# Kernel optimization log

Hardware: AMD Instinct MI355X
Metric: run time of the kernel (lower is better)

Reference implementation:

```python
import jax, jax.numpy as jnp
import numpy as np

B, N = 2048, 110
H1, F1 = 5, 24   # gat1: 5 heads, 24-dim, concat
H2, F2 = 3, 3    # gat2: 3 heads, 3-dim, average
NEG = -9e15
ALPHA = 0.2  # tf.nn.leaky_relu default alpha


def _glorot(key, shape):
    fan_in, fan_out = shape[-2], shape[-1]
    lim = np.sqrt(6.0 / (fan_in + fan_out))
    return jax.random.uniform(key, shape, jnp.float32, -lim, lim)


def setup_inputs() -> dict:
    key = jax.random.key(0)
    ks = jax.random.split(key, 12)
    X = jax.random.normal(ks[0], (B, N, N), jnp.float32)
    # sparse-ish 0/1 adjacency with self-loops
    A = (jax.random.uniform(ks[1], (B, N, N)) < 0.3).astype(jnp.float32)
    A = jnp.maximum(A, jnp.eye(N, dtype=jnp.float32)[None])
    return {
        "X": X,
        "A": A,
        "M": jax.random.normal(ks[2], (N, N), jnp.float32),  # learnable mask
        "W1": _glorot(ks[3], (H1, N, F1)),
        "as1": _glorot(ks[4], (H1, F1, 1))[..., 0],
        "an1": _glorot(ks[5], (H1, F1, 1))[..., 0],
        "b1": jnp.zeros((F1,), jnp.float32),
        "W2": _glorot(ks[6], (H2, H1 * F1, F2)),
        "as2": _glorot(ks[7], (H2, F2, 1))[..., 0],
        "an2": _glorot(ks[8], (H2, F2, 1))[..., 0],
        "b2": jnp.zeros((F2,), jnp.float32),
        "fc1_w": _glorot(ks[9], (F2, 1)),
        "fc2_w": _glorot(ks[10], (N, N)),
    }


def _gat_layer(X, A, W, a_s, a_n, b, concat):
    # X: [B,N,Din]; W: [H,Din,F]; a_s,a_n: [H,F]; b: [F]
    feats = jnp.einsum('bni,hif->bhnf', X, W)               # per-head projection
    e_s = jnp.einsum('bhnf,hf->bhn', feats, a_s)
    e_n = jnp.einsum('bhnf,hf->bhn', feats, a_n)
    e = jax.nn.leaky_relu(e_s[..., :, None] + e_n[..., None, :], ALPHA)  # [B,H,N,N]
    e = jnp.where(A[:, None] > 0.0, e, NEG)                  # adjacency mask
    attn = jax.nn.softmax(e, axis=-1)
    h = jnp.einsum('bhnm,bhmf->bhnf', attn, feats) + b       # aggregate + bias
    if concat:
        h = jax.nn.leaky_relu(h, ALPHA)
        b_, hh, n_, f_ = h.shape
        return h.transpose(0, 2, 1, 3).reshape(b_, n_, hh * f_)
    # 'average': add heads / H, then activation
    return jax.nn.leaky_relu(h.mean(axis=1), ALPHA)


def reference(X, A, M, W1, as1, an1, b1, W2, as2, an2, b2, fc1_w, fc2_w):
    Xm = X * jax.nn.sigmoid(M)[None]                         # learnable mask gating
    h1 = _gat_layer(Xm, A, W1, as1, an1, b1, concat=True)    # [B,N,H1*F1]
    h2 = _gat_layer(h1, A, W2, as2, an2, b2, concat=False)   # [B,N,F2]
    node_prob = jax.nn.sigmoid(h2 @ fc1_w)                   # [B,N,1]
    t = node_prob.reshape(-1, N)                             # [B,N]
    attn_prob = jax.nn.softmax(t @ fc2_w, axis=-1)           # [B,N]
    return jnp.sum(t * attn_prob, axis=1, keepdims=True)     # [B,1]
```

## Files before the change

### kernel.cpp

```cpp
#include <hip/hip_runtime.h>
#include <math.h>

#define NB 2048
#define NV 110
#define NH1 5
#define NF1 24
#define NH2 3
#define NF2 3
#define C1 (NH1*NF1)
#define LALPHA 0.2f

constexpr int NN = NV*NV;
constexpr int T1 = 512;
constexpr int KP = 136;
constexpr int W1ROWS = 144;

typedef _Float16 f16;
typedef f16  f16x8 __attribute__((ext_vector_type(8)));
typedef f16  f16x4 __attribute__((ext_vector_type(4)));
typedef __fp16 h16x2 __attribute__((ext_vector_type(2)));
typedef float f32x4 __attribute__((ext_vector_type(4)));

__device__ __forceinline__ f32x4 mfma16(f16x8 a, f16x8 b, f32x4 c) {
  return __builtin_amdgcn_mfma_f32_16x16x32_f16(a, b, c, 0, 0, 0);
}
__device__ __forceinline__ float lrelu(float x){ return x > 0.f ? x : LALPHA*x; }
__device__ __forceinline__ float frcp(float x){ return __builtin_amdgcn_rcpf(x); }
__device__ __forceinline__ float sigm(float x){ return frcp(1.f+__expf(-x)); }
__device__ __forceinline__ float expm4(float v){
  return __builtin_amdgcn_exp2f(fmaf(v, 1.442695041f, -5.770780163f));
}
__device__ __forceinline__ float wmax(float v){
  #pragma unroll
  for (int d=32; d; d>>=1) v = fmaxf(v, __shfl_xor(v,d));
  return v;
}
__device__ __forceinline__ float wsum(float v){
  #pragma unroll
  for (int d=32; d; d>>=1) v += __shfl_xor(v,d);
  return v;
}
__device__ __forceinline__ f32x4 ld4u(const float* p){
  f32x4 v; __builtin_memcpy(&v, p, 16); return v;
}

__global__ void precomp_kernel(const float* __restrict__ M, const float* __restrict__ W1,
                               const float* __restrict__ as1, const float* __restrict__ an1,
                               const float* __restrict__ W2, const float* __restrict__ as2,
                               const float* __restrict__ an2, const float* __restrict__ fc2w,
                               float* __restrict__ Msig, f16* __restrict__ W1tg,
                               f16* __restrict__ W2tg, f16* __restrict__ fc2tg) {
  const int i = blockIdx.x*256 + threadIdx.x;
  if (i < NN) {
    Msig[i] = sigm(M[i]);
  } else if (i < NN + W1ROWS*KP) {
    const int j = i - NN, f = j/KP, k = j%KP;
    float v = 0.f;
    if (k < NV) {
      if (f < C1) {
        v = W1[(f/NF1)*(NV*NF1) + k*NF1 + (f%NF1)];
      } else if (f >= 128 && f < 133) {
        const int h = f - 128;
        for (int ff = 0; ff < NF1; ++ff)
          v += W1[h*(NV*NF1) + k*NF1 + ff] * as1[h*NF1 + ff];
      } else if (f >= 133 && f < 138) {
        const int h = f - 133;
        for (int ff = 0; ff < NF1; ++ff)
          v += W1[h*(NV*NF1) + k*NF1 + ff] * an1[h*NF1 + ff];
      }
    }
    W1tg[f*KP + k] = (f16)v;
  } else if (i < NN + W1ROWS*KP + 16*KP) {
    const int j = i - NN - W1ROWS*KP, r = j/KP, k = j%KP;
    float v = 0.f;
    if (k < C1) {
      if (r < 9) {
        v = W2[(r/NF2)*(C1*NF2) + k*NF2 + (r%NF2)];
      } else if (r < 12) {
        const int g = r - 9;
        for (int f2 = 0; f2 < NF2; ++f2)
          v += W2[g*(C1*NF2) + k*NF2 + f2] * as2[g*NF2 + f2];
      } else if (r < 15) {
        const int g = r - 12;
        for (int f2 = 0; f2 < NF2; ++f2)
          v += W2[g*(C1*NF2) + k*NF2 + f2] * an2[g*NF2 + f2];
      }
    }
    W2tg[r*KP + k] = (f16)v;
  } else if (i < NN + W1ROWS*KP + 16*KP + 112*KP) {
    const int j = i - NN - W1ROWS*KP - 16*KP, col = j/KP, k = j%KP;
    float v = 0.f;
    if (col < NV && k < NV) v = fc2w[k*NV + col];
    fc2tg[col*KP + k] = (f16)v;
  }
}

__global__ __launch_bounds__(T1, 4) void gat_fused(
  const float* __restrict__ X, const float* __restrict__ A,
  const float* __restrict__ Msig, const f16* __restrict__ W1tg,
  const float* __restrict__ b1,  const f16* __restrict__ W2tg,
  const float* __restrict__ b2,  const float* __restrict__ fc1w,
  const f16* __restrict__ fc2tg, float* __restrict__ out)
{
  __shared__ __attribute__((aligned(16))) f16 sXm [112*KP];
  __shared__ __attribute__((aligned(16))) f16 sFt [128*KP];
  __shared__ __attribute__((aligned(16))) f16 sF2t[16*KP];
  __shared__ __attribute__((aligned(16))) float sES [NH1*112];
  __shared__ __attribute__((aligned(16))) float sEN [NH1*128];
  __shared__ __attribute__((aligned(16))) float sES2[NH2*112];
  __shared__ __attribute__((aligned(16))) float sEN2[NH2*128];
  __shared__ unsigned long long sAM[2*112];

  const int b = blockIdx.x, tid = threadIdx.x;
  const int wv = tid >> 6, lane = tid & 63;
  const int lr = lane & 15, lh = lane >> 4;
  const float* __restrict__ Xb = X + (size_t)b*NN;
  const float* __restrict__ Ab = A + (size_t)b*NN;

  float* const sT = sES;
  float* const sS = sES + 128;

  for (int n = tid; n < 110; n += T1) {
    *(unsigned*)&sXm[n*KP + 110] = 0u;
    *(uint4*)&sXm[n*KP + 112] = uint4{0,0,0,0};
    *(uint4*)&sXm[n*KP + 120] = uint4{0,0,0,0};
    *(uint4*)&sXm[n*KP + 128] = uint4{0,0,0,0};
  }
  for (int i = tid; i < 2*KP/8; i += T1)
    ((uint4*)&sXm[110*KP])[i] = uint4{0,0,0,0};
  for (int n = tid; n < 128; n += T1) {
    *(uint4*)&sFt[n*KP + 112] = uint4{0,0,0,0};
    *(uint4*)&sFt[n*KP + 120] = uint4{0,0,0,0};
    *(uint4*)&sFt[n*KP + 128] = uint4{0,0,0,0};
  }
  for (int i = tid; i < (16*KP)/8; i += T1)
    ((uint4*)sF2t)[i] = uint4{0,0,0,0};
  if (tid < 4) sAM[220 + tid] = 0ull;

  for (int t = tid; t < NV*28; t += T1) {
    const int n = t/28, c = t%28, k = 4*c;
    if (c < 27) {
      f32x4 x = ld4u(Xb + n*NV + k);
      f32x4 m = ld4u(Msig + n*NV + k);
      union { f16x4 v4; h16x2 h2[2]; } u;
      u.h2[0] = __builtin_amdgcn_cvt_pkrtz(x[0]*m[0], x[1]*m[1]);
      u.h2[1] = __builtin_amdgcn_cvt_pkrtz(x[2]*m[2], x[3]*m[3]);
      *(f16x4*)&sXm[n*KP + k] = u.v4;
    } else {
      sXm[n*KP + 108] = (f16)(Xb[n*NV+108]*Msig[n*NV+108]);
      sXm[n*KP + 109] = (f16)(Xb[n*NV+109]*Msig[n*NV+109]);
    }
  }
  #pragma unroll
  for (int i = 0; i < 14; ++i) {
    const int n = wv + 8*i;
    if (n < NV) {
      unsigned long long m0 = __ballot(Ab[n*NV + lane] > 0.f);
      const int mm = 64 + lane;
      unsigned long long m1 = __ballot((mm < NV) && (Ab[n*NV + mm] > 0.f));
      if (lane == 0) { sAM[2*n] = m0; sAM[2*n+1] = m1; }
    }
  }
  f16x8 bW[4], bL[4];
  #pragma unroll
  for (int k = 0; k < 4; ++k)
    bW[k] = *(const f16x8*)&W1tg[(wv*16 + lr)*KP + k*32 + lh*8];
  if (wv < 2) {
    #pragma unroll
    for (int k = 0; k < 4; ++k)
      bL[k] = *(const f16x8*)&W1tg[(128 + lr)*KP + k*32 + lh*8];
  }
  __syncthreads();

  #pragma unroll
  for (int m = 0; m < 7; ++m) {
    f32x4 acc = {0.f,0.f,0.f,0.f};
    #pragma unroll
    for (int k = 0; k < 4; ++k) {
      f16x8 af = *(const f16x8*)&sXm[(m*16 + lr)*KP + k*32 + lh*8];
      acc = mfma16(af, bW[k], acc);
    }
    f16x4 v;
    #pragma unroll
    for (int r = 0; r < 4; ++r) v[r] = (f16)acc[r];
    *(f16x4*)&sFt[(wv*16 + lr)*KP + m*16 + lh*4] = v;
  }
  if (wv < 2) {
    const int mlo = wv ? 4 : 0, mhi = wv ? 7 : 4;
    for (int m = mlo; m < mhi; ++m) {
      f32x4 acc = {0.f,0.f,0.f,0.f};
      #pragma unroll
      for (int k = 0; k < 4; ++k) {
        f16x8 af = *(const f16x8*)&sXm[(m*16 + lr)*KP + k*32 + lh*8];
        acc = mfma16(af, bL[k], acc);
      }
      const int mg0 = m*16 + lh*4;
      if (lr < 5)       *(f32x4*)&sES[lr*112 + mg0] = acc;
      else if (lr < 10) *(f32x4*)&sEN[(lr-5)*128 + mg0] = acc;
    }
  }
  __syncthreads();

  const int row  = wv*16 + lr;
  const int arow = (row < 112) ? row : 0;
  const unsigned long long am0 = sAM[2*arow], am1 = sAM[2*arow+1];
  const float bvt0 = (lr < NF1) ? b1[lr] : 0.f;
  const float bvt1 = (16 + lr < NF1) ? b1[16 + lr] : 0.f;

  f16 h1r[5][2][4];
  f16x8 pa[4];
  if (wv < 7) {
    #pragma unroll
    for (int p = 0; p < 5; ++p) {
      const float es = sES[p*112 + row];
      float psum = 0.f;
      #pragma unroll
      for (int k = 0; k < 4; ++k) {
        const int cb = k*32 + lh*8;
        const f32x4 enA = *(const f32x4*)&sEN[p*128 + cb];
        const f32x4 enB = *(const f32x4*)&sEN[p*128 + cb + 4];
        const unsigned bits = (unsigned)(((cb & 64) ? am1 : am0) >> (cb & 63)) & 0xFFu;
        float e[8];
        #pragma unroll
        for (int j = 0; j < 8; ++j) {
          float v = es + ((j < 4) ? enA[j] : enB[j-4]);
          v = fmaxf(v, LALPHA*v);
          v = (bits & (1u << j)) ? v : -1e30f;
          e[j] = expm4(v);
        }
        psum += ((e[0]+e[1]) + (e[2]+e[3])) + ((e[4]+e[5]) + (e[6]+e[7]));
        union { f16x8 v8; h16x2 h2[4]; } u;
        u.h2[0] = __builtin_amdgcn_cvt_pkrtz(e[0], e[1]);
        u.h2[1] = __builtin_amdgcn_cvt_pkrtz(e[2], e[3]);
        u.h2[2] = __builtin_amdgcn_cvt_pkrtz(e[4], e[5]);
        u.h2[3] = __builtin_amdgcn_cvt_pkrtz(e[6], e[7]);
        pa[k] = u.v8;
      }
      psum += __shfl_xor(psum, 16);
      psum += __shfl_xor(psum, 32);
      f32x4 rs;
      #pragma unroll
      for (int r = 0; r < 4; ++r) rs[r] = __shfl(psum, lh*4 + r);
      #pragma unroll
      for (int nt2 = 0; nt2 < 2; ++nt2) {
        f32x4 acc = {0.f,0.f,0.f,0.f};
        #pragma unroll
        for (int k = 0; k < 4; ++k) {
          f16x8 bf = *(const f16x8*)&sFt[(p*NF1 + nt2*16 + lr)*KP + k*32 + lh*8];
          acc = mfma16(pa[k], bf, acc);
        }
        const float bv = nt2 ? bvt1 : bvt0;
        #pragma unroll
        for (int r = 0; r < 4; ++r)
          h1r[p][nt2][r] = (f16)lrelu(acc[r]*frcp(rs[r]) + bv);
      }
    }
    #pragma unroll
    for (int p = 0; p < 5; ++p) {
      #pragma unroll
      for (int nt2 = 0; nt2 < 2; ++nt2) {
        const int fl = nt2*16 + lr;
        if (fl < NF1) {
          #pragma unroll
          for (int r = 0; r < 4; ++r) {
            const int mg = wv*16 + lh*4 + r;
            if (mg < NV) sXm[mg*KP + p*NF1 + fl] = h1r[p][nt2][r];
          }
        }
      }
    }
    {
      f32x4 acc = {0.f,0.f,0.f,0.f};
      #pragma unroll
      for (int k = 0; k < 4; ++k) {
        f16x8 af = *(const f16x8*)&sXm[(wv*16 + lr)*KP + k*32 + lh*8];
        f16x8 bf = *(const f16x8*)&W2tg[lr*KP + k*32 + lh*8];
        acc = mfma16(af, bf, acc);
      }
      const int mg0 = wv*16 + lh*4;
      if (lr < 9) {
        #pragma unroll
        for (int r = 0; r < 4; ++r) {
          const int mg = mg0 + r;
          if (mg < NV) sF2t[lr*KP + mg] = (f16)acc[r];
        }
      } else if (lr < 12) {
        *(f32x4*)&sES2[(lr-9)*112 + mg0] = acc;
      } else if (lr < 15) {
        *(f32x4*)&sEN2[(lr-12)*128 + mg0] = acc;
      }
    }
  }
  __syncthreads();

  f32x4 a2_0 = {0.f,0.f,0.f,0.f};
  f32x4 a2_1 = {0.f,0.f,0.f,0.f};
  f32x4 a2_2 = {0.f,0.f,0.f,0.f};
  float ps0 = 0.f, ps1 = 0.f, ps2 = 0.f;
  if (wv == 7) {
    if (lane < 18) sT[110 + lane] = 0.f;
  }
  if (wv < 7) {
    #pragma unroll
    for (int g = 0; g < 3; ++g) {
      const float es = sES2[g*112 + row];
      float psum = 0.f;
      #pragma unroll
      for (int k = 0; k < 4; ++k) {
        const int cb = k*32 + lh*8;
        const f32x4 enA = *(const f32x4*)&sEN2[g*128 + cb];
        const f32x4 enB = *(const f32x4*)&sEN2[g*128 + cb + 4];
        const unsigned bits = (unsigned)(((cb & 64) ? am1 : am0) >> (cb & 63)) & 0xFFu;
        float e[8];
        #pragma unroll
        for (int j = 0; j < 8; ++j) {
          float v = es + ((j < 4) ? enA[j] : enB[j-4]);
          v = fmaxf(v, LALPHA*v);
          v = (bits & (1u << j)) ? v : -1e30f;
          e[j] = expm4(v);
        }
        psum += ((e[0]+e[1]) + (e[2]+e[3])) + ((e[4]+e[5]) + (e[6]+e[7]));
        union { f16x8 v8; h16x2 h2[4]; } u;
        u.h2[0] = __builtin_amdgcn_cvt_pkrtz(e[0], e[1]);
        u.h2[1] = __builtin_amdgcn_cvt_pkrtz(e[2], e[3]);
        u.h2[2] = __builtin_amdgcn_cvt_pkrtz(e[4], e[5]);
        u.h2[3] = __builtin_amdgcn_cvt_pkrtz(e[6], e[7]);
        pa[k] = u.v8;
      }
      psum += __shfl_xor(psum, 16);
      psum += __shfl_xor(psum, 32);
      if (g == 0) ps0 = psum; else if (g == 1) ps1 = psum; else ps2 = psum;
      const int brow = (lr < NF2) ? (g*NF2 + lr) : 15;
      #pragma unroll
      for (int k = 0; k < 4; ++k) {
        f16x8 bf = *(const f16x8*)&sF2t[brow*KP + k*32 + lh*8];
        if (g == 0)      a2_0 = mfma16(pa[k], bf, a2_0);
        else if (g == 1) a2_1 = mfma16(pa[k], bf, a2_1);
        else             a2_2 = mfma16(pa[k], bf, a2_2);
      }
    }
    const float fcv = (lr < NF2) ? fc1w[lr] : 0.f;
    const float b2v = (lr < NF2) ? b2[lr]  : 0.f;
    #pragma unroll
    for (int r = 0; r < 4; ++r) {
      const int src = lh*4 + r;
      const float rs0 = __shfl(ps0, src);
      const float rs1 = __shfl(ps1, src);
      const float rs2 = __shfl(ps2, src);
      const float hsum = a2_0[r]*frcp(rs0) + a2_1[r]*frcp(rs1)
                       + a2_2[r]*frcp(rs2);
      float hv = (lr < NF2) ? lrelu(hsum*(1.f/NH2) + b2v)*fcv : 0.f;
      hv += __shfl_xor(hv, 1);
      hv += __shfl_xor(hv, 2);
      hv += __shfl_xor(hv, 4);
      hv += __shfl_xor(hv, 8);
      if (lr == 0) {
        const int mg = wv*16 + lh*4 + r;
        if (mg < NV) sT[mg] = sigm(hv);
      }
    }
  }
  __syncthreads();
  if (wv < 7) {
    f32x4 acc = {0.f,0.f,0.f,0.f};
    #pragma unroll
    for (int k = 0; k < 4; ++k) {
      const int cb = k*32 + lh*8;
      const f32x4 tA = *(const f32x4*)&sT[cb];
      const f32x4 tB = *(const f32x4*)&sT[cb + 4];
      union { f16x8 v8; h16x2 h2[4]; } u;
      u.h2[0] = __builtin_amdgcn_cvt_pkrtz(tA[0], tA[1]);
      u.h2[1] = __builtin_amdgcn_cvt_pkrtz(tA[2], tA[3]);
      u.h2[2] = __builtin_amdgcn_cvt_pkrtz(tB[0], tB[1]);
      u.h2[3] = __builtin_amdgcn_cvt_pkrtz(tB[2], tB[3]);
      f16x8 bf = *(const f16x8*)&fc2tg[(wv*16 + lr)*KP + k*32 + lh*8];
      acc = mfma16(u.v8, bf, acc);
    }
    const int col = wv*16 + lr;
    if (lh == 0 && col < NV) sS[col] = acc[0];
  }
  __syncthreads();
  if (wv == 0) {
    const float s0 = sS[lane];
    const float s1 = (64+lane < NV) ? sS[64+lane] : -1e38f;
    const float mx = wmax(fmaxf(s0, s1));
    const float p0 = __expf(s0 - mx);
    const float p1 = (64+lane < NV) ? __expf(s1 - mx) : 0.f;
    const float sum = wsum(p0 + p1);
    float val = sT[lane]*p0 + ((64+lane < NV) ? sT[64+lane]*p1 : 0.f);
    val = wsum(val);
    if (lane == 0) out[b] = val*frcp(sum);
  }
}

extern "C" void kernel_launch(void* const* d_in, const int* in_sizes, int n_in,
                              void* d_out, int out_size, void* d_ws, size_t ws_size,
                              hipStream_t stream) {
  const float* X   = (const float*)d_in[0];
  const float* A   = (const float*)d_in[1];
  const float* M   = (const float*)d_in[2];
  const float* W1  = (const float*)d_in[3];
  const float* as1 = (const float*)d_in[4];
  const float* an1 = (const float*)d_in[5];
  const float* b1  = (const float*)d_in[6];
  const float* W2  = (const float*)d_in[7];
  const float* as2 = (const float*)d_in[8];
  const float* an2 = (const float*)d_in[9];
  const float* b2  = (const float*)d_in[10];
  const float* fc1 = (const float*)d_in[11];
  const float* fc2 = (const float*)d_in[12];
  float* out = (float*)d_out;

  float* Msig = (float*)d_ws;
  f16* W1tg  = (f16*)((char*)d_ws + 48400);
  f16* W2tg  = (f16*)((char*)d_ws + 48400 + W1ROWS*KP*2);
  f16* fc2tg = (f16*)((char*)d_ws + 48400 + W1ROWS*KP*2 + 16*KP*2);

  const int pre_items = NN + W1ROWS*KP + 16*KP + 112*KP;
  precomp_kernel<<<(pre_items + 255)/256, 256, 0, stream>>>(
      M, W1, as1, an1, W2, as2, an2, fc2, Msig, W1tg, W2tg, fc2tg);
  gat_fused<<<NB, T1, 0, stream>>>(X, A, Msig, W1tg, b1, W2tg,
                                   b2, fc1, fc2tg, out);
}
```

Measured before the change: 150.0 us.

## Double block to 16 waves and split heads across two wave halves

Raises the block size from 512 to 1024 threads and splits the work between two groups of 8 waves. The first GEMM's row tiles, the layer-1 heads (3 vs 2) and the layer-2 heads (2 vs 1) are divided between the groups. Partial layer-2 head outputs go through a new shared buffer, and an extra barrier separates the layer-1 aggregation from the layer-2 projection. The goal is more parallelism per batch item with fewer serial head iterations per wave. The cost is extra synchronisation and register pressure at 1024 threads per block, and fewer resident blocks per CU.

```diff
diff --git a/kernel.cpp b/kernel.cpp
--- a/kernel.cpp
+++ b/kernel.cpp
@@ -11,7 +11,7 @@
 #define LALPHA 0.2f
 
 constexpr int NN = NV*NV;
-constexpr int T1 = 512;
+constexpr int T1 = 1024;
 constexpr int KP = 136;
 constexpr int W1ROWS = 144;
 
@@ -95,7 +95,7 @@
   }
 }
 
-__global__ __launch_bounds__(T1, 4) void gat_fused(
+__global__ __launch_bounds__(T1, 8) void gat_fused(
   const float* __restrict__ X, const float* __restrict__ A,
   const float* __restrict__ Msig, const f16* __restrict__ W1tg,
   const float* __restrict__ b1,  const f16* __restrict__ W2tg,
@@ -110,9 +110,11 @@
   __shared__ __attribute__((aligned(16))) float sES2[NH2*112];
   __shared__ __attribute__((aligned(16))) float sEN2[NH2*128];
   __shared__ unsigned long long sAM[2*112];
+  __shared__ __attribute__((aligned(16))) float sHP[112*4];
 
   const int b = blockIdx.x, tid = threadIdx.x;
   const int wv = tid >> 6, lane = tid & 63;
+  const int wq = wv & 7, half = wv >> 3;
   const int lr = lane & 15, lh = lane >> 4;
   const float* __restrict__ Xb = X + (size_t)b*NN;
   const float* __restrict__ Ab = A + (size_t)b*NN;
@@ -152,8 +154,8 @@
     }
   }
   #pragma unroll
-  for (int i = 0; i < 14; ++i) {
-    const int n = wv + 8*i;
+  for (int i = 0; i < 7; ++i) {
+    const int n = wv + 16*i;
     if (n < NV) {
       unsigned long long m0 = __ballot(Ab[n*NV + lane] > 0.f);
       const int mm = 64 + lane;
@@ -164,204 +166,221 @@
   f16x8 bW[4], bL[4];
   #pragma unroll
   for (int k = 0; k < 4; ++k)
-    bW[k] = *(const f16x8*)&W1tg[(wv*16 + lr)*KP + k*32 + lh*8];
-  if (wv < 2) {
+    bW[k] = *(const f16x8*)&W1tg[(wq*16 + lr)*KP + k*32 + lh*8];
+  if (half && wq < 7) {
     #pragma unroll
     for (int k = 0; k < 4; ++k)
       bL[k] = *(const f16x8*)&W1tg[(128 + lr)*KP + k*32 + lh*8];
   }
   __syncthreads();
 
-  #pragma unroll
-  for (int m = 0; m < 7; ++m) {
-    f32x4 acc = {0.f,0.f,0.f,0.f};
-    #pragma unroll
-    for (int k = 0; k < 4; ++k) {
-      f16x8 af = *(const f16x8*)&sXm[(m*16 + lr)*KP + k*32 + lh*8];
-      acc = mfma16(af, bW[k], acc);
-    }
-    f16x4 v;
-    #pragma unroll
-    for (int r = 0; r < 4; ++r) v[r] = (f16)acc[r];
-    *(f16x4*)&sFt[(wv*16 + lr)*KP + m*16 + lh*4] = v;
-  }
-  if (wv < 2) {
-    const int mlo = wv ? 4 : 0, mhi = wv ? 7 : 4;
+  {
+    const int mlo = half ? 4 : 0, mhi = half ? 7 : 4;
     for (int m = mlo; m < mhi; ++m) {
       f32x4 acc = {0.f,0.f,0.f,0.f};
       #pragma unroll
       for (int k = 0; k < 4; ++k) {
         f16x8 af = *(const f16x8*)&sXm[(m*16 + lr)*KP + k*32 + lh*8];
+        acc = mfma16(af, bW[k], acc);
+      }
+      f16x4 v;
+      #pragma unroll
+      for (int r = 0; r < 4; ++r) v[r] = (f16)acc[r];
+      *(f16x4*)&sFt[(wq*16 + lr)*KP + m*16 + lh*4] = v;
+    }
+    if (half && wq < 7) {
+      f32x4 acc = {0.f,0.f,0.f,0.f};
+      #pragma unroll
+      for (int k = 0; k < 4; ++k) {
+        f16x8 af = *(const f16x8*)&sXm[(wq*16 + lr)*KP + k*32 + lh*8];
         acc = mfma16(af, bL[k], acc);
       }
-      const int mg0 = m*16 + lh*4;
+      const int mg0 = wq*16 + lh*4;
       if (lr < 5)       *(f32x4*)&sES[lr*112 + mg0] = acc;
       else if (lr < 10) *(f32x4*)&sEN[(lr-5)*128 + mg0] = acc;
     }
   }
   __syncthreads();
 
-  const int row  = wv*16 + lr;
+  const int row  = wq*16 + lr;
   const int arow = (row < 112) ? row : 0;
   const unsigned long long am0 = sAM[2*arow], am1 = sAM[2*arow+1];
   const float bvt0 = (lr < NF1) ? b1[lr] : 0.f;
   const float bvt1 = (16 + lr < NF1) ? b1[16 + lr] : 0.f;
-
-  f16 h1r[5][2][4];
+  const int np = half ? 2 : 3, pbase = half ? 3 : 0;
+
+  f16 h1r[3][2][4];
   f16x8 pa[4];
-  if (wv < 7) {
-    #pragma unroll
-    for (int p = 0; p < 5; ++p) {
-      const float es = sES[p*112 + row];
-      float psum = 0.f;
-      #pragma unroll
-      for (int k = 0; k < 4; ++k) {
-        const int cb = k*32 + lh*8;
-        const f32x4 enA = *(const f32x4*)&sEN[p*128 + cb];
-        const f32x4 enB = *(const f32x4*)&sEN[p*128 + cb + 4];
-        const unsigned bits = (unsigned)(((cb & 64) ? am1 : am0) >> (cb & 63)) & 0xFFu;
-        float e[8];
-        #pragma unroll
-        for (int j = 0; j < 8; ++j) {
-          float v = es + ((j < 4) ? enA[j] : enB[j-4]);
-          v = fmaxf(v, LALPHA*v);
-          v = (bits & (1u << j)) ? v : -1e30f;
-          e[j] = expm4(v);
+  if (wq < 7) {
+    #pragma unroll
+    for (int pi = 0; pi < 3; ++pi) {
+      if (pi < np) {
+        const int p = pbase + pi;
+        const float es = sES[p*112 + row];
+        float psum = 0.f;
+        #pragma unroll
+        for (int k = 0; k < 4; ++k) {
+          const int cb = k*32 + lh*8;
+          const f32x4 enA = *(const f32x4*)&sEN[p*128 + cb];
+          const f32x4 enB = *(const f32x4*)&sEN[p*128 + cb + 4];
+          const unsigned bits = (unsigned)(((cb & 64) ? am1 : am0) >> (cb & 63)) & 0xFFu;
+          float e[8];
+          #pragma unroll
+          for (int j = 0; j < 8; ++j) {
+            float v = es + ((j < 4) ? enA[j] : enB[j-4]);
+            v = fmaxf(v, LALPHA*v);
+            v = (bits & (1u << j)) ? v : -1e30f;
+            e[j] = expm4(v);
+          }
+          psum += ((e[0]+e[1]) + (e[2]+e[3])) + ((e[4]+e[5]) + (e[6]+e[7]));
+          union { f16x8 v8; h16x2 h2[4]; } u;
+          u.h2[0] = __builtin_amdgcn_cvt_pkrtz(e[0], e[1]);
+          u.h2[1] = __builtin_amdgcn_cvt_pkrtz(e[2], e[3]);
+          u.h2[2] = __builtin_amdgcn_cvt_pkrtz(e[4], e[5]);
+          u.h2[3] = __builtin_amdgcn_cvt_pkrtz(e[6], e[7]);
+          pa[k] = u.v8;
         }
-        psum += ((e[0]+e[1]) + (e[2]+e[3])) + ((e[4]+e[5]) + (e[6]+e[7]));
-        union { f16x8 v8; h16x2 h2[4]; } u;
-        u.h2[0] = __builtin_amdgcn_cvt_pkrtz(e[0], e[1]);
-        u.h2[1] = __builtin_amdgcn_cvt_pkrtz(e[2], e[3]);
-        u.h2[2] = __builtin_amdgcn_cvt_pkrtz(e[4], e[5]);
-        u.h2[3] = __builtin_amdgcn_cvt_pkrtz(e[6], e[7]);
-        pa[k] = u.v8;
-      }
-      psum += __shfl_xor(psum, 16);
-      psum += __shfl_xor(psum, 32);
-      f32x4 rs;
-      #pragma unroll
-      for (int r = 0; r < 4; ++r) rs[r] = __shfl(psum, lh*4 + r);
-      #pragma unroll
-      for (int nt2 = 0; nt2 < 2; ++nt2) {
-        f32x4 acc = {0.f,0.f,0.f,0.f};
-        #pragma unroll
-        for (int k = 0; k < 4; ++k) {
-          f16x8 bf = *(const f16x8*)&sFt[(p*NF1 + nt2*16 + lr)*KP + k*32 + lh*8];
-          acc = mfma16(pa[k], bf, acc);
+        psum += __shfl_xor(psum, 16);
+        psum += __shfl_xor(psum, 32);
+        f32x4 rs;
+        #pragma unroll
+        for (int r = 0; r < 4; ++r) rs[r] = __shfl(psum, lh*4 + r);
+        #pragma unroll
+        for (int nt2 = 0; nt2 < 2; ++nt2) {
+          f32x4 acc = {0.f,0.f,0.f,0.f};
+          #pragma unroll
+          for (int k = 0; k < 4; ++k) {
+            f16x8 bf = *(const f16x8*)&sFt[(p*NF1 + nt2*16 + lr)*KP + k*32 + lh*8];
+            acc = mfma16(pa[k], bf, acc);
+          }
+          const float bv = nt2 ? bvt1 : bvt0;
+          #pragma unroll
+          for (int r = 0; r < 4; ++r)
+            h1r[pi][nt2][r] = (f16)lrelu(acc[r]*frcp(rs[r]) + bv);
         }
-        const float bv = nt2 ? bvt1 : bvt0;
-        #pragma unroll
-        for (int r = 0; r < 4; ++r)
-          h1r[p][nt2][r] = (f16)lrelu(acc[r]*frcp(rs[r]) + bv);
-      }
-    }
-    #pragma unroll
-    for (int p = 0; p < 5; ++p) {
-      #pragma unroll
-      for (int nt2 = 0; nt2 < 2; ++nt2) {
-        const int fl = nt2*16 + lr;
-        if (fl < NF1) {
-          #pragma unroll
-          for (int r = 0; r < 4; ++r) {
-            const int mg = wv*16 + lh*4 + r;
-            if (mg < NV) sXm[mg*KP + p*NF1 + fl] = h1r[p][nt2][r];
+      }
+    }
+    #pragma unroll
+    for (int pi = 0; pi < 3; ++pi) {
+      if (pi < np) {
+        const int p = pbase + pi;
+        #pragma unroll
+        for (int nt2 = 0; nt2 < 2; ++nt2) {
+          const int fl = nt2*16 + lr;
+          if (fl < NF1) {
+            #pragma unroll
+            for (int r = 0; r < 4; ++r) {
+              const int mg = wq*16 + lh*4 + r;
+              if (mg < NV) sXm[mg*KP + p*NF1 + fl] = h1r[pi][nt2][r];
+            }
           }
         }
       }
     }
-    {
-      f32x4 acc = {0.f,0.f,0.f,0.f};
+  }
+  __syncthreads();
+
+  if (!half && wq < 7) {
+    f32x4 acc = {0.f,0.f,0.f,0.f};
+    #pragma unroll
+    for (int k = 0; k < 4; ++k) {
+      f16x8 af = *(const f16x8*)&sXm[(wq*16 + lr)*KP + k*32 + lh*8];
+      f16x8 bf = *(const f16x8*)&W2tg[lr*KP + k*32 + lh*8];
+      acc = mfma16(af, bf, acc);
+    }
+    const int mg0 = wq*16 + lh*4;
+    if (lr < 9) {
       #pragma unroll
-      for (int k = 0; k < 4; ++k) {
-        f16x8 af = *(const f16x8*)&sXm[(wv*16 + lr)*KP + k*32 + lh*8];
-        f16x8 bf = *(const f16x8*)&W2tg[lr*KP + k*32 + lh*8];
-        acc = mfma16(af, bf, acc);
-      }
-      const int mg0 = wv*16 + lh*4;
-      if (lr < 9) {
-        #pragma unroll
-        for (int r = 0; r < 4; ++r) {
-          const int mg = mg0 + r;
-          if (mg < NV) sF2t[lr*KP + mg] = (f16)acc[r];
+      for (int r = 0; r < 4; ++r) {
+        const int mg = mg0 + r;
+        if (mg < NV) sF2t[lr*KP + mg] = (f16)acc[r];
+      }
+    } else if (lr < 12) {
+      *(f32x4*)&sES2[(lr-9)*112 + mg0] = acc;
+    } else if (lr < 15) {
+      *(f32x4*)&sEN2[(lr-12)*128 + mg0] = acc;
+    }
+  }
+  __syncthreads();
+
+  f32x4 a2A = {0.f,0.f,0.f,0.f};
+  f32x4 a2B = {0.f,0.f,0.f,0.f};
+  float psA = 0.f, psB = 0.f;
+  const int ng = half ? 1 : 2, gbase = half ? 2 : 0;
+  if (wv == 15 && lane < 18) sT[110 + lane] = 0.f;
+  if (wq < 7) {
+    #pragma unroll
+    for (int gi = 0; gi < 2; ++gi) {
+      if (gi < ng) {
+        const int g = gbase + gi;
+        const float es = sES2[g*112 + row];
+        float psum = 0.f;
+        #pragma unroll
+        for (int k = 0; k < 4; ++k) {
+          const int cb = k*32 + lh*8;
+          const f32x4 enA = *(const f32x4*)&sEN2[g*128 + cb];
+          const f32x4 enB = *(const f32x4*)&sEN2[g*128 + cb + 4];
+          const unsigned bits = (unsigned)(((cb & 64) ? am1 : am0) >> (cb & 63)) & 0xFFu;
+          float e[8];
+          #pragma unroll
+          for (int j = 0; j < 8; ++j) {
+            float v = es + ((j < 4) ? enA[j] : enB[j-4]);
+            v = fmaxf(v, LALPHA*v);
+            v = (bits & (1u << j)) ? v : -1e30f;
+            e[j] = expm4(v);
+          }
+          psum += ((e[0]+e[1]) + (e[2]+e[3])) + ((e[4]+e[5]) + (e[6]+e[7]));
+          union { f16x8 v8; h16x2 h2[4]; } u;
+          u.h2[0] = __builtin_amdgcn_cvt_pkrtz(e[0], e[1]);
+          u.h2[1] = __builtin_amdgcn_cvt_pkrtz(e[2], e[3]);
+          u.h2[2] = __builtin_amdgcn_cvt_pkrtz(e[4], e[5]);
+          u.h2[3] = __builtin_amdgcn_cvt_pkrtz(e[6], e[7]);
+          pa[k] = u.v8;
         }
-      } else if (lr < 12) {
-        *(f32x4*)&sES2[(lr-9)*112 + mg0] = acc;
-      } else if (lr < 15) {
-        *(f32x4*)&sEN2[(lr-12)*128 + mg0] = acc;
-      }
-    }
-  }
-  __syncthreads();
-
-  f32x4 a2_0 = {0.f,0.f,0.f,0.f};
-  f32x4 a2_1 = {0.f,0.f,0.f,0.f};
-  f32x4 a2_2 = {0.f,0.f,0.f,0.f};
-  float ps0 = 0.f, ps1 = 0.f, ps2 = 0.f;
-  if (wv == 7) {
-    if (lane < 18) sT[110 + lane] = 0.f;
-  }
-  if (wv < 7) {
-    #pragma unroll
-    for (int g = 0; g < 3; ++g) {
-      const float es = sES2[g*112 + row];
-      float psum = 0.f;
-      #pragma unroll
-      for (int k = 0; k < 4; ++k) {
-        const int cb = k*32 + lh*8;
-        const f32x4 enA = *(const f32x4*)&sEN2[g*128 + cb];
-        const f32x4 enB = *(const f32x4*)&sEN2[g*128 + cb + 4];
-        const unsigned bits = (unsigned)(((cb & 64) ? am1 : am0) >> (cb & 63)) & 0xFFu;
-        float e[8];
-        #pragma unroll
-        for (int j = 0; j < 8; ++j) {
-          float v = es + ((j < 4) ? enA[j] : enB[j-4]);
-          v = fmaxf(v, LALPHA*v);
-          v = (bits & (1u << j)) ? v : -1e30f;
-          e[j] = expm4(v);
+        psum += __shfl_xor(psum, 16);
+        psum += __shfl_xor(psum, 32);
+        if (gi == 0) psA = psum; else psB = psum;
+        const int brow = (lr < NF2) ? (g*NF2 + lr) : 15;
+        #pragma unroll
+        for (int k = 0; k < 4; ++k) {
+          f16x8 bf = *(const f16x8*)&sF2t[brow*KP + k*32 + lh*8];
+          if (gi == 0) a2A = mfma16(pa[k], bf, a2A);
+          else         a2B = mfma16(pa[k], bf, a2B);
         }
-        psum += ((e[0]+e[1]) + (e[2]+e[3])) + ((e[4]+e[5]) + (e[6]+e[7]));
-        union { f16x8 v8; h16x2 h2[4]; } u;
-        u.h2[0] = __builtin_amdgcn_cvt_pkrtz(e[0], e[1]);
-        u.h2[1] = __builtin_amdgcn_cvt_pkrtz(e[2], e[3]);
-        u.h2[2] = __builtin_amdgcn_cvt_pkrtz(e[4], e[5]);
-        u.h2[3] = __builtin_amdgcn_cvt_pkrtz(e[6], e[7]);
-        pa[k] = u.v8;
-      }
-      psum += __shfl_xor(psum, 16);
-      psum += __shfl_xor(psum, 32);
-      if (g == 0) ps0 = psum; else if (g == 1) ps1 = psum; else ps2 = psum;
-      const int brow = (lr < NF2) ? (g*NF2 + lr) : 15;
-      #pragma unroll
-      for (int k = 0; k < 4; ++k) {
-        f16x8 bf = *(const f16x8*)&sF2t[brow*KP + k*32 + lh*8];
-        if (g == 0)      a2_0 = mfma16(pa[k], bf, a2_0);
-        else if (g == 1) a2_1 = mfma16(pa[k], bf, a2_1);
-        else             a2_2 = mfma16(pa[k], bf, a2_2);
-      }
-    }
+      }
+    }
+  }
+  if (half && wq < 7) {
+    #pragma unroll
+    for (int r = 0; r < 4; ++r) {
+      const int mg = wq*16 + lh*4 + r;
+      const float rs2 = __shfl(psA, lh*4 + r);
+      if (lr < NF2 && mg < NV) sHP[mg*4 + lr] = a2A[r]*frcp(rs2);
+    }
+  }
+  __syncthreads();
+
+  if (!half && wq < 7) {
     const float fcv = (lr < NF2) ? fc1w[lr] : 0.f;
     const float b2v = (lr < NF2) ? b2[lr]  : 0.f;
     #pragma unroll
     for (int r = 0; r < 4; ++r) {
-      const int src = lh*4 + r;
-      const float rs0 = __shfl(ps0, src);
-      const float rs1 = __shfl(ps1, src);
-      const float rs2 = __shfl(ps2, src);
-      const float hsum = a2_0[r]*frcp(rs0) + a2_1[r]*frcp(rs1)
-                       + a2_2[r]*frcp(rs2);
+      const int mg = wq*16 + lh*4 + r;
+      const float rs0 = __shfl(psA, lh*4 + r);
+      const float rs1 = __shfl(psB, lh*4 + r);
+      float hsum = a2A[r]*frcp(rs0) + a2B[r]*frcp(rs1);
+      if (lr < NF2 && mg < NV) hsum += sHP[mg*4 + lr];
       float hv = (lr < NF2) ? lrelu(hsum*(1.f/NH2) + b2v)*fcv : 0.f;
       hv += __shfl_xor(hv, 1);
       hv += __shfl_xor(hv, 2);
       hv += __shfl_xor(hv, 4);
       hv += __shfl_xor(hv, 8);
-      if (lr == 0) {
-        const int mg = wv*16 + lh*4 + r;
-        if (mg < NV) sT[mg] = sigm(hv);
-      }
-    }
-  }
-  __syncthreads();
-  if (wv < 7) {
+      if (lr == 0 && mg < NV) sT[mg] = sigm(hv);
+    }
+  }
+  __syncthreads();
+
+  if (!half && wq < 7) {
     f32x4 acc = {0.f,0.f,0.f,0.f};
     #pragma unroll
     for (int k = 0; k < 4; ++k) {
@@ -373,10 +392,10 @@
       u.h2[1] = __builtin_amdgcn_cvt_pkrtz(tA[2], tA[3]);
       u.h2[2] = __builtin_amdgcn_cvt_pkrtz(tB[0], tB[1]);
       u.h2[3] = __builtin_amdgcn_cvt_pkrtz(tB[2], tB[3]);
-      f16x8 bf = *(const f16x8*)&fc2tg[(wv*16 + lr)*KP + k*32 + lh*8];
+      f16x8 bf = *(const f16x8*)&fc2tg[(wq*16 + lr)*KP + k*32 + lh*8];
       acc = mfma16(u.v8, bf, acc);
     }
-    const int col = wv*16 + lr;
+    const int col = wq*16 + lr;
     if (lh == 0 && col < NV) sS[col] = acc[0];
   }
   __syncthreads();
```

Result: slower. 182.5 us (+21.7%).

## Use 12 waves and distribute GAT head/tile work items across all waves

Applied to the files above, without the earlier changes.

Raises the block to 768 threads (12 waves) and turns the fixed per-wave loops into strided work-item loops over (feature tile, row tile) and (head, row tile) pairs. Layer-1 projection, layer-1 attention per head, and layer-2 attention per head are now spread over all waves instead of 7–8. Layer-1 outputs are written straight to shared memory rather than held in registers, and layer-2 per-head partials go through a shared buffer aliased onto sFt. This adds a __syncthreads and extra shared-memory traffic, and the larger block with launch bounds of 6 blocks may limit registers and occupancy.

```diff
diff --git a/kernel.cpp b/kernel.cpp
--- a/kernel.cpp
+++ b/kernel.cpp
@@ -11,7 +11,7 @@
 #define LALPHA 0.2f
 
 constexpr int NN = NV*NV;
-constexpr int T1 = 512;
+constexpr int T1 = 768;
 constexpr int KP = 136;
 constexpr int W1ROWS = 144;
 
@@ -95,7 +95,7 @@
   }
 }
 
-__global__ __launch_bounds__(T1, 4) void gat_fused(
+__global__ __launch_bounds__(T1, 6) void gat_fused(
   const float* __restrict__ X, const float* __restrict__ A,
   const float* __restrict__ Msig, const f16* __restrict__ W1tg,
   const float* __restrict__ b1,  const f16* __restrict__ W2tg,
@@ -119,6 +119,7 @@
 
   float* const sT = sES;
   float* const sS = sES + 128;
+  float* const sHPf = (float*)sFt;
 
   for (int n = tid; n < 110; n += T1) {
     *(unsigned*)&sXm[n*KP + 110] = 0u;
@@ -152,8 +153,8 @@
     }
   }
   #pragma unroll
-  for (int i = 0; i < 14; ++i) {
-    const int n = wv + 8*i;
+  for (int i = 0; i < 10; ++i) {
+    const int n = wv + 12*i;
     if (n < NV) {
       unsigned long long m0 = __ballot(Ab[n*NV + lane] > 0.f);
       const int mm = 64 + lane;
@@ -161,206 +162,188 @@
       if (lane == 0) { sAM[2*n] = m0; sAM[2*n+1] = m1; }
     }
   }
-  f16x8 bW[4], bL[4];
-  #pragma unroll
-  for (int k = 0; k < 4; ++k)
-    bW[k] = *(const f16x8*)&W1tg[(wv*16 + lr)*KP + k*32 + lh*8];
-  if (wv < 2) {
+  __syncthreads();
+
+  #pragma unroll 1
+  for (int j = wv; j < 63; j += 12) {
+    const int ft = j/7, m = j%7;
+    const int brow = (ft < 8) ? (ft*16 + lr) : (128 + lr);
+    f16x8 bf[4];
     #pragma unroll
     for (int k = 0; k < 4; ++k)
-      bL[k] = *(const f16x8*)&W1tg[(128 + lr)*KP + k*32 + lh*8];
-  }
-  __syncthreads();
-
-  #pragma unroll
-  for (int m = 0; m < 7; ++m) {
+      bf[k] = *(const f16x8*)&W1tg[brow*KP + k*32 + lh*8];
     f32x4 acc = {0.f,0.f,0.f,0.f};
     #pragma unroll
     for (int k = 0; k < 4; ++k) {
       f16x8 af = *(const f16x8*)&sXm[(m*16 + lr)*KP + k*32 + lh*8];
-      acc = mfma16(af, bW[k], acc);
-    }
-    f16x4 v;
-    #pragma unroll
-    for (int r = 0; r < 4; ++r) v[r] = (f16)acc[r];
-    *(f16x4*)&sFt[(wv*16 + lr)*KP + m*16 + lh*4] = v;
-  }
-  if (wv < 2) {
-    const int mlo = wv ? 4 : 0, mhi = wv ? 7 : 4;
-    for (int m = mlo; m < mhi; ++m) {
+      acc = mfma16(af, bf[k], acc);
+    }
+    if (ft < 8) {
+      f16x4 v;
+      #pragma unroll
+      for (int r = 0; r < 4; ++r) v[r] = (f16)acc[r];
+      *(f16x4*)&sFt[(ft*16 + lr)*KP + m*16 + lh*4] = v;
+    } else {
+      const int mg0 = m*16 + lh*4;
+      if (lr < 5)       *(f32x4*)&sES[lr*112 + mg0] = acc;
+      else if (lr < 10) *(f32x4*)&sEN[(lr-5)*128 + mg0] = acc;
+    }
+  }
+  __syncthreads();
+
+  const float bvt0 = (lr < NF1) ? b1[lr] : 0.f;
+  const float bvt1 = (16 + lr < NF1) ? b1[16 + lr] : 0.f;
+
+  f16x8 pa[4];
+  #pragma unroll 1
+  for (int j = wv; j < 35; j += 12) {
+    const int p = j/7, m = j%7;
+    const int row = m*16 + lr;
+    const unsigned long long am0 = sAM[2*row], am1 = sAM[2*row+1];
+    const float es = sES[p*112 + row];
+    float psum = 0.f;
+    #pragma unroll
+    for (int k = 0; k < 4; ++k) {
+      const int cb = k*32 + lh*8;
+      const f32x4 enA = *(const f32x4*)&sEN[p*128 + cb];
+      const f32x4 enB = *(const f32x4*)&sEN[p*128 + cb + 4];
+      const unsigned bits = (unsigned)(((cb & 64) ? am1 : am0) >> (cb & 63)) & 0xFFu;
+      float e[8];
+      #pragma unroll
+      for (int jj = 0; jj < 8; ++jj) {
+        float v = es + ((jj < 4) ? enA[jj] : enB[jj-4]);
+        v = fmaxf(v, LALPHA*v);
+        v = (bits & (1u << jj)) ? v : -1e30f;
+        e[jj] = expm4(v);
+      }
+      psum += ((e[0]+e[1]) + (e[2]+e[3])) + ((e[4]+e[5]) + (e[6]+e[7]));
+      union { f16x8 v8; h16x2 h2[4]; } u;
+      u.h2[0] = __builtin_amdgcn_cvt_pkrtz(e[0], e[1]);
+      u.h2[1] = __builtin_amdgcn_cvt_pkrtz(e[2], e[3]);
+      u.h2[2] = __builtin_amdgcn_cvt_pkrtz(e[4], e[5]);
+      u.h2[3] = __builtin_amdgcn_cvt_pkrtz(e[6], e[7]);
+      pa[k] = u.v8;
+    }
+    psum += __shfl_xor(psum, 16);
+    psum += __shfl_xor(psum, 32);
+    f32x4 rs;
+    #pragma unroll
+    for (int r = 0; r < 4; ++r) rs[r] = __shfl(psum, lh*4 + r);
+    #pragma unroll
+    for (int nt2 = 0; nt2 < 2; ++nt2) {
       f32x4 acc = {0.f,0.f,0.f,0.f};
       #pragma unroll
       for (int k = 0; k < 4; ++k) {
-        f16x8 af = *(const f16x8*)&sXm[(m*16 + lr)*KP + k*32 + lh*8];
-        acc = mfma16(af, bL[k], acc);
-      }
-      const int mg0 = m*16 + lh*4;
-      if (lr < 5)       *(f32x4*)&sES[lr*112 + mg0] = acc;
-      else if (lr < 10) *(f32x4*)&sEN[(lr-5)*128 + mg0] = acc;
-    }
-  }
-  __syncthreads();
-
-  const int row  = wv*16 + lr;
-  const int arow = (row < 112) ? row : 0;
-  const unsigned long long am0 = sAM[2*arow], am1 = sAM[2*arow+1];
-  const float bvt0 = (lr < NF1) ? b1[lr] : 0.f;
-  const float bvt1 = (16 + lr < NF1) ? b1[16 + lr] : 0.f;
-
-  f16 h1r[5][2][4];
-  f16x8 pa[4];
-  if (wv < 7) {
-    #pragma unroll
-    for (int p = 0; p < 5; ++p) {
-      const float es = sES[p*112 + row];
-      float psum = 0.f;
-      #pragma unroll
-      for (int k = 0; k < 4; ++k) {
-        const int cb = k*32 + lh*8;
-        const f32x4 enA = *(const f32x4*)&sEN[p*128 + cb];
-        const f32x4 enB = *(const f32x4*)&sEN[p*128 + cb + 4];
-        const unsigned bits = (unsigned)(((cb & 64) ? am1 : am0) >> (cb & 63)) & 0xFFu;
-        float e[8];
-        #pragma unroll
-        for (int j = 0; j < 8; ++j) {
-          float v = es + ((j < 4) ? enA[j] : enB[j-4]);
-          v = fmaxf(v, LALPHA*v);
-          v = (bits & (1u << j)) ? v : -1e30f;
-          e[j] = expm4(v);
-        }
-        psum += ((e[0]+e[1]) + (e[2]+e[3])) + ((e[4]+e[5]) + (e[6]+e[7]));
-        union { f16x8 v8; h16x2 h2[4]; } u;
-        u.h2[0] = __builtin_amdgcn_cvt_pkrtz(e[0], e[1]);
-        u.h2[1] = __builtin_amdgcn_cvt_pkrtz(e[2], e[3]);
-        u.h2[2] = __builtin_amdgcn_cvt_pkrtz(e[4], e[5]);
-        u.h2[3] = __builtin_amdgcn_cvt_pkrtz(e[6], e[7]);
-        pa[k] = u.v8;
-      }
-      psum += __shfl_xor(psum, 16);
-      psum += __shfl_xor(psum, 32);
-      f32x4 rs;
-      #pragma unroll
-      for (int r = 0; r < 4; ++r) rs[r] = __shfl(psum, lh*4 + r);
-      #pragma unroll
-      for (int nt2 = 0; nt2 < 2; ++nt2) {
-        f32x4 acc = {0.f,0.f,0.f,0.f};
-        #pragma unroll
-        for (int k = 0; k < 4; ++k) {
-          f16x8 bf = *(const f16x8*)&sFt[(p*NF1 + nt2*16 + lr)*KP + k*32 + lh*8];
-          acc = mfma16(pa[k], bf, acc);
-        }
-        const float bv = nt2 ? bvt1 : bvt0;
-        #pragma unroll
-        for (int r = 0; r < 4; ++r)
-          h1r[p][nt2][r] = (f16)lrelu(acc[r]*frcp(rs[r]) + bv);
-      }
-    }
-    #pragma unroll
-    for (int p = 0; p < 5; ++p) {
-      #pragma unroll
-      for (int nt2 = 0; nt2 < 2; ++nt2) {
-        const int fl = nt2*16 + lr;
-        if (fl < NF1) {
-          #pragma unroll
-          for (int r = 0; r < 4; ++r) {
-            const int mg = wv*16 + lh*4 + r;
-            if (mg < NV) sXm[mg*KP + p*NF1 + fl] = h1r[p][nt2][r];
-          }
-        }
-      }
-    }
-    {
-      f32x4 acc = {0.f,0.f,0.f,0.f};
-      #pragma unroll
-      for (int k = 0; k < 4; ++k) {
-        f16x8 af = *(const f16x8*)&sXm[(wv*16 + lr)*KP + k*32 + lh*8];
-        f16x8 bf = *(const f16x8*)&W2tg[lr*KP + k*32 + lh*8];
-        acc = mfma16(af, bf, acc);
-      }
-      const int mg0 = wv*16 + lh*4;
-      if (lr < 9) {
+        f16x8 bf = *(const f16x8*)&sFt[(p*NF1 + nt2*16 + lr)*KP + k*32 + lh*8];
+        acc = mfma16(pa[k], bf, acc);
+      }
+      const int fl = nt2*16 + lr;
+      const float bv = nt2 ? bvt1 : bvt0;
+      if (fl < NF1) {
         #pragma unroll
         for (int r = 0; r < 4; ++r) {
-          const int mg = mg0 + r;
-          if (mg < NV) sF2t[lr*KP + mg] = (f16)acc[r];
+          const int mg = m*16 + lh*4 + r;
+          if (mg < NV)
+            sXm[mg*KP + p*NF1 + fl] = (f16)lrelu(acc[r]*frcp(rs[r]) + bv);
         }
-      } else if (lr < 12) {
-        *(f32x4*)&sES2[(lr-9)*112 + mg0] = acc;
-      } else if (lr < 15) {
-        *(f32x4*)&sEN2[(lr-12)*128 + mg0] = acc;
-      }
-    }
-  }
-  __syncthreads();
-
-  f32x4 a2_0 = {0.f,0.f,0.f,0.f};
-  f32x4 a2_1 = {0.f,0.f,0.f,0.f};
-  f32x4 a2_2 = {0.f,0.f,0.f,0.f};
-  float ps0 = 0.f, ps1 = 0.f, ps2 = 0.f;
-  if (wv == 7) {
-    if (lane < 18) sT[110 + lane] = 0.f;
-  }
+      }
+    }
+  }
+  __syncthreads();
+
   if (wv < 7) {
-    #pragma unroll
-    for (int g = 0; g < 3; ++g) {
-      const float es = sES2[g*112 + row];
-      float psum = 0.f;
+    f32x4 acc = {0.f,0.f,0.f,0.f};
+    #pragma unroll
+    for (int k = 0; k < 4; ++k) {
+      f16x8 af = *(const f16x8*)&sXm[(wv*16 + lr)*KP + k*32 + lh*8];
+      f16x8 bf = *(const f16x8*)&W2tg[lr*KP + k*32 + lh*8];
+      acc = mfma16(af, bf, acc);
+    }
+    const int mg0 = wv*16 + lh*4;
+    if (lr < 9) {
       #pragma unroll
-      for (int k = 0; k < 4; ++k) {
-        const int cb = k*32 + lh*8;
-        const f32x4 enA = *(const f32x4*)&sEN2[g*128 + cb];
-        const f32x4 enB = *(const f32x4*)&sEN2[g*128 + cb + 4];
-        const unsigned bits = (unsigned)(((cb & 64) ? am1 : am0) >> (cb & 63)) & 0xFFu;
-        float e[8];
-        #pragma unroll
-        for (int j = 0; j < 8; ++j) {
-          float v = es + ((j < 4) ? enA[j] : enB[j-4]);
-          v = fmaxf(v, LALPHA*v);
-          v = (bits & (1u << j)) ? v : -1e30f;
-          e[j] = expm4(v);
-        }
-        psum += ((e[0]+e[1]) + (e[2]+e[3])) + ((e[4]+e[5]) + (e[6]+e[7]));
-        union { f16x8 v8; h16x2 h2[4]; } u;
-        u.h2[0] = __builtin_amdgcn_cvt_pkrtz(e[0], e[1]);
-        u.h2[1] = __builtin_amdgcn_cvt_pkrtz(e[2], e[3]);
-        u.h2[2] = __builtin_amdgcn_cvt_pkrtz(e[4], e[5]);
-        u.h2[3] = __builtin_amdgcn_cvt_pkrtz(e[6], e[7]);
-        pa[k] = u.v8;
-      }
-      psum += __shfl_xor(psum, 16);
-      psum += __shfl_xor(psum, 32);
-      if (g == 0) ps0 = psum; else if (g == 1) ps1 = psum; else ps2 = psum;
-      const int brow = (lr < NF2) ? (g*NF2 + lr) : 15;
+      for (int r = 0; r < 4; ++r) {
+        const int mg = mg0 + r;
+        if (mg < NV) sF2t[lr*KP + mg] = (f16)acc[r];
+      }
+    } else if (lr < 12) {
+      *(f32x4*)&sES2[(lr-9)*112 + mg0] = acc;
+    } else if (lr < 15) {
+      *(f32x4*)&sEN2[(lr-12)*128 + mg0] = acc;
+    }
+  }
+  __syncthreads();
+
+  #pragma unroll 1
+  for (int j = wv; j < 21; j += 12) {
+    const int g = j/7, m = j%7;
+    const int row = m*16 + lr;
+    const unsigned long long am0 = sAM[2*row], am1 = sAM[2*row+1];
+    const float es = sES2[g*112 + row];
+    float psum = 0.f;
+    #pragma unroll
+    for (int k = 0; k < 4; ++k) {
+      const int cb = k*32 + lh*8;
+      const f32x4 enA = *(const f32x4*)&sEN2[g*128 + cb];
+      const f32x4 enB = *(const f32x4*)&sEN2[g*128 + cb + 4];
+      const unsigned bits = (unsigned)(((cb & 64) ? am1 : am0) >> (cb & 63)) & 0xFFu;
+      float e[8];
       #pragma unroll
-      for (int k = 0; k < 4; ++k) {
-        f16x8 bf = *(const f16x8*)&sF2t[brow*KP + k*32 + lh*8];
-        if (g == 0)      a2_0 = mfma16(pa[k], bf, a2_0);
-        else if (g == 1) a2_1 = mfma16(pa[k], bf, a2_1);
-        else             a2_2 = mfma16(pa[k], bf, a2_2);
-      }
-    }
+      for (int jj = 0; jj < 8; ++jj) {
+        float v = es + ((jj < 4) ? enA[jj] : enB[jj-4]);
+        v = fmaxf(v, LALPHA*v);
+        v = (bits & (1u << jj)) ? v : -1e30f;
+        e[jj] = expm4(v);
+      }
+      psum += ((e[0]+e[1]) + (e[2]+e[3])) + ((e[4]+e[5]) + (e[6]+e[7]));
+      union { f16x8 v8; h16x2 h2[4]; } u;
+      u.h2[0] = __builtin_amdgcn_cvt_pkrtz(e[0], e[1]);
+      u.h2[1] = __builtin_amdgcn_cvt_pkrtz(e[2], e[3]);
+      u.h2[2] = __builtin_amdgcn_cvt_pkrtz(e[4], e[5]);
+      u.h2[3] = __builtin_amdgcn_cvt_pkrtz(e[6], e[7]);
+      pa[k] = u.v8;
+    }
+    psum += __shfl_xor(psum, 16);
+    psum += __shfl_xor(psum, 32);
+    f32x4 rs;
+    #pragma unroll
+    for (int r = 0; r < 4; ++r) rs[r] = __shfl(psum, lh*4 + r);
+    const int brow = (lr < NF2) ? (g*NF2 + lr) : 15;
+    f32x4 acc = {0.f,0.f,0.f,0.f};
+    #pragma unroll
+    for (int k = 0; k < 4; ++k) {
+      f16x8 bf = *(const f16x8*)&sF2t[brow*KP + k*32 + lh*8];
+      acc = mfma16(pa[k], bf, acc);
+    }
+    #pragma unroll
+    for (int r = 0; r < 4; ++r) {
+      const int mg = m*16 + lh*4 + r;
+      if (lr < NF2 && mg < NV)
+        sHPf[g*448 + mg*4 + lr] = acc[r]*frcp(rs[r]);
+    }
+  }
+  if (wv == 11 && lane < 18) sT[110 + lane] = 0.f;
+  __syncthreads();
+
+  if (wv < 7) {
     const float fcv = (lr < NF2) ? fc1w[lr] : 0.f;
     const float b2v = (lr < NF2) ? b2[lr]  : 0.f;
     #pragma unroll
     for (int r = 0; r < 4; ++r) {
-      const int src = lh*4 + r;
-      const float rs0 = __shfl(ps0, src);
-      const float rs1 = __shfl(ps1, src);
-      const float rs2 = __shfl(ps2, src);
-      const float hsum = a2_0[r]*frcp(rs0) + a2_1[r]*frcp(rs1)
-                       + a2_2[r]*frcp(rs2);
+      const int mg = wv*16 + lh*4 + r;
+      float hsum = 0.f;
+      if (lr < NF2 && mg < NV)
+        hsum = sHPf[mg*4 + lr] + sHPf[448 + mg*4 + lr] + sHPf[896 + mg*4 + lr];
       float hv = (lr < NF2) ? lrelu(hsum*(1.f/NH2) + b2v)*fcv : 0.f;
       hv += __shfl_xor(hv, 1);
       hv += __shfl_xor(hv, 2);
       hv += __shfl_xor(hv, 4);
       hv += __shfl_xor(hv, 8);
-      if (lr == 0) {
-        const int mg = wv*16 + lh*4 + r;
-        if (mg < NV) sT[mg] = sigm(hv);
-      }
-    }
-  }
-  __syncthreads();
+      if (lr == 0 && mg < NV) sT[mg] = sigm(hv);
+    }
+  }
+  __syncthreads();
+
   if (wv < 7) {
     f32x4 acc = {0.f,0.f,0.f,0.f};
     #pragma unroll
```

Measured after the change: 157.2 us. 4.8% more time.
